# Kernel tuning notes

Measured on AMD Instinct MI355X. Metric: run time of the kernel, lower is better.

The kernel has to match this reference:

```python
import jax, jax.numpy as jnp
import numpy as np

B, D, UNITS = 32768, 1024, 1024
NB_FACTOR, SPARSITY = 3, 32
NB = D // SPARSITY  # 32 blocks of 32x32 per block-diagonal factor


def _block_t_matmul(kb, y):
    # kb: [nb, bi, bo] block-diagonal factor values; y: [nb*bi, batch]
    # computes blockdiag(kb)^T @ y without materializing the dense matrix
    nb, bi, bo = kb.shape
    yb = y.reshape(nb, bi, -1)                      # [nb, bi, batch]
    out = jnp.einsum('nio,nib->nob', kb, yb)        # [nb, bo, batch]
    return out.reshape(nb * bo, -1)


def setup_inputs() -> dict:
    key = jax.random.key(0)
    ks = jax.random.split(key, 9)
    return {
        'x': jax.random.normal(ks[0], (B, D), jnp.float32),
        'P0': jax.random.normal(ks[1], (D, D), jnp.float32),
        'P1': jax.random.normal(ks[2], (D, D), jnp.float32),
        'P2': jax.random.normal(ks[3], (D, D), jnp.float32),
        'P3': jax.random.normal(ks[4], (UNITS, UNITS), jnp.float32),
        'K0': jax.random.normal(ks[5], (NB, SPARSITY, SPARSITY), jnp.float32) * 0.05,
        'K1': jax.random.normal(ks[6], (NB, SPARSITY, SPARSITY), jnp.float32) * 0.05,
        'K2': jax.random.normal(ks[7], (NB, SPARSITY, SPARSITY), jnp.float32) * 0.05,
        'bias': jax.random.normal(ks[8], (UNITS,), jnp.float32),
    }


def reference(x, P0, P1, P2, P3, K0, K1, K2, bias):
    # output = (softmax(P3) @ Bd2^T @ softmax(P2) @ Bd1^T @ softmax(P1) @ Bd0^T @ softmax(P0) @ x^T)^T + bias
    y = x.T                                          # [D, B]
    y = jax.nn.softmax(P0, axis=1) @ y
    for kb, perm in ((K0, P1), (K1, P2), (K2, P3)):
        y = _block_t_matmul(kb, y)
        y = jax.nn.softmax(perm, axis=1) @ y
    out = y.T + bias                                 # [B, UNITS]
    return out
```

## Files before the change

kernel.cpp:

```cpp
#include <hip/hip_runtime.h>
#include <hip/hip_bf16.h>

typedef __bf16 bf16x8 __attribute__((ext_vector_type(8)));
typedef float f32x4 __attribute__((ext_vector_type(4)));
typedef unsigned short u16x8 __attribute__((ext_vector_type(8)));

__device__ __forceinline__ unsigned short f2bf(float f) {
  unsigned u = __float_as_uint(f);
  u += 0x7FFF + ((u >> 16) & 1);
  return (unsigned short)(u >> 16);
}
__device__ __forceinline__ float bf2f(unsigned short h) {
  return __uint_as_float((unsigned)h << 16);
}

__device__ __forceinline__ void gload_lds16(const void* g, void* l) {
  __builtin_amdgcn_global_load_lds(
      (const __attribute__((address_space(1))) void*)g,
      (__attribute__((address_space(3))) void*)l, 16, 0, 0);
}

#define LBAR() do { asm volatile("s_waitcnt lgkmcnt(0)" ::: "memory"); \
                    __builtin_amdgcn_s_barrier(); } while (0)

__device__ __forceinline__ void convert_slice(const float* __restrict__ x,
                                              unsigned short* __restrict__ xb,
                                              int base8, int cnt8, int cb, int nb)
{
  int i = cb * 256 + (int)threadIdx.x;
  const int stride = nb * 256;
  for (; i < cnt8; i += stride) {
    const size_t g = (size_t)(base8 + i);
    float4 v0 = ((const float4*)x)[2 * g];
    float4 v1 = ((const float4*)x)[2 * g + 1];
    u16x8 uv;
    uv[0] = f2bf(v0.x); uv[1] = f2bf(v0.y); uv[2] = f2bf(v0.z); uv[3] = f2bf(v0.w);
    uv[4] = f2bf(v1.x); uv[5] = f2bf(v1.y); uv[6] = f2bf(v1.z); uv[7] = f2bf(v1.w);
    ((u16x8*)xb)[g] = uv;
  }
}

__global__ __launch_bounds__(256)
void softmax4_kernel(const float* __restrict__ P0, const float* __restrict__ P1,
                     const float* __restrict__ P2, const float* __restrict__ P3,
                     unsigned short* __restrict__ S,
                     const float* __restrict__ cvx, unsigned short* __restrict__ cvxb,
                     int cvt_cnt)
{
  if (blockIdx.x >= 4096) {
    convert_slice(cvx, cvxb, 0, cvt_cnt, blockIdx.x - 4096, gridDim.x - 4096);
    return;
  }
  const int bid = blockIdx.x;
  const int mat = bid >> 10, row = bid & 1023;
  const float* P = (mat == 0 ? P0 : mat == 1 ? P1 : mat == 2 ? P2 : P3) + (size_t)row * 1024;
  unsigned short* out = S + ((size_t)mat << 20) + (size_t)row * 1024;
  const int t = threadIdx.x, w = t >> 6, l = t & 63;
  float4 v = ((const float4*)P)[t];
  float mx = fmaxf(fmaxf(v.x, v.y), fmaxf(v.z, v.w));
  #pragma unroll
  for (int off = 32; off > 0; off >>= 1) mx = fmaxf(mx, __shfl_xor(mx, off));
  __shared__ float redA[4], redB[4];
  if (l == 0) redA[w] = mx;
  __syncthreads();
  mx = fmaxf(fmaxf(redA[0], redA[1]), fmaxf(redA[2], redA[3]));
  float e0 = __expf(v.x - mx), e1 = __expf(v.y - mx);
  float e2 = __expf(v.z - mx), e3 = __expf(v.w - mx);
  float s = e0 + e1 + e2 + e3;
  #pragma unroll
  for (int off = 32; off > 0; off >>= 1) s += __shfl_xor(s, off);
  if (l == 0) redB[w] = s;
  __syncthreads();
  s = redB[0] + redB[1] + redB[2] + redB[3];
  float inv = 1.0f / s;
  ushort4 o;
  o.x = f2bf(e0 * inv); o.y = f2bf(e1 * inv);
  o.z = f2bf(e2 * inv); o.w = f2bf(e3 * inv);
  ((ushort4*)out)[t] = o;
}

__global__ __launch_bounds__(256)
void blockdiagT_kernel(const float* __restrict__ Kb, const unsigned short* __restrict__ in,
                       unsigned short* __restrict__ outT,
                       const float* __restrict__ cvx, unsigned short* __restrict__ cvxb,
                       int cvt_base, int cvt_cnt)
{
  if (blockIdx.x >= 128) {
    convert_slice(cvx, cvxb, cvt_base, cvt_cnt, blockIdx.x - 128, gridDim.x - 128);
    return;
  }
  const int n = blockIdx.x >> 2;
  const int c = (blockIdx.x & 3) * 256 + threadIdx.x;
  __shared__ float Ks[32][33];
  for (int t = threadIdx.x; t < 1024; t += 256)
    Ks[t >> 5][t & 31] = Kb[n * 1024 + t];
  __syncthreads();
  float ri[32];
  #pragma unroll
  for (int i = 0; i < 32; ++i)
    ri[i] = bf2f(in[(size_t)(n * 32 + i) * 1024 + c]);
  unsigned short ov[32];
  #pragma unroll
  for (int o = 0; o < 32; ++o) {
    float acc = 0.f;
    #pragma unroll
    for (int i = 0; i < 32; ++i) acc = fmaf(Ks[i][o], ri[i], acc);
    ov[o] = f2bf(acc);
  }
  u16x8* dst = (u16x8*)(outT + (size_t)c * 1024 + n * 32);
  const u16x8* src = (const u16x8*)ov;
  #pragma unroll
  for (int q = 0; q < 4; ++q) dst[q] = src[q];
}

template<int TILE, bool A_FP32, bool OUT_BIAS>
__global__ __launch_bounds__(256)
void gemm_bt_kernel(const void* __restrict__ Av, const unsigned short* __restrict__ B,
                    void* __restrict__ Cv, const float* __restrict__ bias,
                    int M, int N, int K, int nprim,
                    const float* cvx, unsigned short* cvxb, int cvt_base, int cvt_cnt)
{
  if ((int)blockIdx.x >= nprim) {
    convert_slice(cvx, cvxb, cvt_base, cvt_cnt, blockIdx.x - nprim, gridDim.x - nprim);
    return;
  }
  constexpr int FR  = TILE / 32;
  constexpr int SIT = TILE / 32;
  __shared__ unsigned short Asm[TILE * 64];
  __shared__ unsigned short Bsm[TILE * 64];
  const int tid = threadIdx.x;
  const int w = tid >> 6, l = tid & 63;
  const int bid = blockIdx.x;
  const int cpx = nprim >> 3;
  const int swz = (bid & 7) * cpx + (bid >> 3);
  const int ntn = N / TILE;
  const int n0 = (swz % ntn) * TILE;
  const int m0 = (swz / ntn) * TILE;
  const int wr = (w >> 1) * (TILE / 2), wc = (w & 1) * (TILE / 2);
  const int lr = l & 15, kg = (l >> 4) << 3;

  f32x4 acc[FR][FR] = {};
  const int KT = K >> 6;
  for (int kt = 0; kt < KT; ++kt) {
    const int k0 = kt << 6;
    if (kt) __syncthreads();
    #pragma unroll
    for (int it = 0; it < SIT; ++it) {
      int li = it * 256 + tid;
      int row = li >> 3, c8 = (li & 7) << 3;
      const unsigned short* g = B + (size_t)(n0 + row) * K + (k0 + c8);
      gload_lds16(g, (char*)Bsm + it * 4096 + w * 1024);
    }
    if (A_FP32) {
      const float* Af = (const float*)Av;
      #pragma unroll
      for (int p = 0; p < SIT; ++p) {
        int row = (tid >> 3) + p * 32;
        int c8 = (tid & 7) << 3;
        const float* g = Af + (size_t)(m0 + row) * K + (k0 + c8);
        float4 v0 = ((const float4*)g)[0];
        float4 v1 = ((const float4*)g)[1];
        u16x8 uv;
        uv[0] = f2bf(v0.x); uv[1] = f2bf(v0.y); uv[2] = f2bf(v0.z); uv[3] = f2bf(v0.w);
        uv[4] = f2bf(v1.x); uv[5] = f2bf(v1.y); uv[6] = f2bf(v1.z); uv[7] = f2bf(v1.w);
        *(u16x8*)&Asm[row * 64 + c8] = uv;
      }
    } else {
      const unsigned short* Ab = (const unsigned short*)Av;
      #pragma unroll
      for (int it = 0; it < SIT; ++it) {
        int li = it * 256 + tid;
        int row = li >> 3, c8 = (li & 7) << 3;
        const unsigned short* g = Ab + (size_t)(m0 + row) * K + (k0 + c8);
        gload_lds16(g, (char*)Asm + it * 4096 + w * 1024);
      }
    }
    __syncthreads();
    #pragma unroll
    for (int ks = 0; ks < 2; ++ks) {
      const int kb = ks * 32 + kg;
      bf16x8 af[FR], bfr[FR];
      #pragma unroll
      for (int i = 0; i < FR; ++i)
        af[i] = *(const bf16x8*)&Asm[(wr + i * 16 + lr) * 64 + kb];
      #pragma unroll
      for (int j = 0; j < FR; ++j)
        bfr[j] = *(const bf16x8*)&Bsm[(wc + j * 16 + lr) * 64 + kb];
      #pragma unroll
      for (int i = 0; i < FR; ++i)
        #pragma unroll
        for (int j = 0; j < FR; ++j)
          acc[i][j] = __builtin_amdgcn_mfma_f32_16x16x32_bf16(af[i], bfr[j], acc[i][j], 0, 0, 0);
    }
  }
  const int cr = (l >> 4) << 2;
  const int cc = l & 15;
  if (OUT_BIAS) {
    float* C = (float*)Cv;
    #pragma unroll
    for (int j = 0; j < FR; ++j) {
      int col = n0 + wc + j * 16 + cc;
      float bv = bias[col];
      #pragma unroll
      for (int i = 0; i < FR; ++i) {
        int rbase = m0 + wr + i * 16 + cr;
        #pragma unroll
        for (int r = 0; r < 4; ++r)
          C[(size_t)(rbase + r) * N + col] = acc[i][j][r] + bv;
      }
    }
  } else {
    unsigned short* C = (unsigned short*)Cv;
    #pragma unroll
    for (int j = 0; j < FR; ++j) {
      int col = n0 + wc + j * 16 + cc;
      #pragma unroll
      for (int i = 0; i < FR; ++i) {
        int rbase = m0 + wr + i * 16 + cr;
        #pragma unroll
        for (int r = 0; r < 4; ++r)
          C[(size_t)(rbase + r) * N + col] = f2bf(acc[i][j][r]);
      }
    }
  }
}

template<int QI, int QJ>
__device__ __forceinline__ void phase_compute(const char* Ab, const char* Bb,
    int wm, int wn, int lr, int klo, int sw, f32x4 (&accq)[4][2])
{
  const char* Ah = Ab + QI * 16384;
  const char* Bh = Bb + QJ * 16384;
  #pragma unroll
  for (int ks = 0; ks < 2; ++ks) {
    const int cb = (ks * 64 + klo) ^ sw;
    bf16x8 av[4], bv[2];
    #pragma unroll
    for (int i = 0; i < 4; ++i) {
      const int ra = wm * 64 + i * 16 + lr;
      av[i] = *(const bf16x8*)(Ah + ra * 128 + cb);
    }
    #pragma unroll
    for (int j = 0; j < 2; ++j) {
      const int rb = wn * 32 + j * 16 + lr;
      bv[j] = *(const bf16x8*)(Bh + rb * 128 + cb);
    }
    __builtin_amdgcn_s_setprio(1);
    #pragma unroll
    for (int i = 0; i < 4; ++i)
      #pragma unroll
      for (int j = 0; j < 2; ++j)
        accq[i][j] = __builtin_amdgcn_mfma_f32_16x16x32_bf16(av[i], bv[j], accq[i][j], 0, 0, 0);
    __builtin_amdgcn_s_setprio(0);
  }
}

__global__ __launch_bounds__(512, 2)
void gemm256_kernel(const unsigned short* __restrict__ A,
                    const unsigned short* __restrict__ B,
                    float* __restrict__ C, const float* __restrict__ bias,
                    int N, int K)
{
  extern __shared__ __align__(16) char lds[];
  const int tid = threadIdx.x;
  const int w = tid >> 6, l = tid & 63;
  const int wm = w >> 2, wn = w & 3;
  const int lr = l & 15;
  const int klo = (l >> 4) << 4;
  const int sw  = (lr & 7) << 4;

  const int nwg = gridDim.x;
  const int bid = blockIdx.x;
  const int cpx = nwg >> 3;
  const int swz = (bid & 7) * cpx + (bid >> 3);
  const int ntn = N >> 8;
  const int n0 = (swz % ntn) << 8;
  const int m0 = (swz / ntn) << 8;

  unsigned int aoff[2][2], boff[2][2];
  #pragma unroll
  for (int q = 0; q < 2; ++q)
    #pragma unroll
    for (int it = 0; it < 2; ++it) {
      int L = it * 8192 + tid * 16;
      int r = L >> 7;
      int cs = (L & 127) ^ ((r & 7) << 4);
      aoff[q][it] = (unsigned)(m0 + q * 128 + r) * K + (cs >> 1);
      boff[q][it] = (unsigned)(n0 + q * 128 + r) * K + (cs >> 1);
    }
  char* ldsA = lds;
  char* ldsB = lds + 65536;
  const int wdst = w * 1024;

#define STG_A(bufo, q, k0) do { \
    gload_lds16(A + aoff[q][0] + (k0), ldsA + (bufo) + (q) * 16384 + wdst); \
    gload_lds16(A + aoff[q][1] + (k0), ldsA + (bufo) + (q) * 16384 + 8192 + wdst); } while (0)
#define STG_B(bufo, q, k0) do { \
    gload_lds16(B + boff[q][0] + (k0), ldsB + (bufo) + (q) * 16384 + wdst); \
    gload_lds16(B + boff[q][1] + (k0), ldsB + (bufo) + (q) * 16384 + 8192 + wdst); } while (0)

  f32x4 acc[2][2][4][2] = {};

  STG_A(0, 0, 0); STG_B(0, 0, 0); STG_B(0, 1, 0); STG_A(0, 1, 0);

  const int NT = K >> 6;
  int curo = 0;
  for (int t = 0; t < NT - 1; ++t) {
    const int nxto = curo ^ 32768;
    const int k1 = (t + 1) << 6;
    STG_A(nxto, 0, k1);
    asm volatile("s_waitcnt vmcnt(6)" ::: "memory");
    LBAR();
    phase_compute<0, 0>(ldsA + curo, ldsB + curo, wm, wn, lr, klo, sw, acc[0][0]);
    STG_B(nxto, 0, k1);
    asm volatile("s_waitcnt vmcnt(6)" ::: "memory");
    LBAR();
    phase_compute<0, 1>(ldsA + curo, ldsB + curo, wm, wn, lr, klo, sw, acc[0][1]);
    STG_B(nxto, 1, k1);
    asm volatile("s_waitcnt vmcnt(6)" ::: "memory");
    LBAR();
    phase_compute<1, 0>(ldsA + curo, ldsB + curo, wm, wn, lr, klo, sw, acc[1][0]);
    STG_A(nxto, 1, k1);
    phase_compute<1, 1>(ldsA + curo, ldsB + curo, wm, wn, lr, klo, sw, acc[1][1]);
    curo = nxto;
  }
  asm volatile("s_waitcnt vmcnt(4)" ::: "memory");
  LBAR();
  phase_compute<0, 0>(ldsA + curo, ldsB + curo, wm, wn, lr, klo, sw, acc[0][0]);
  asm volatile("s_waitcnt vmcnt(2)" ::: "memory");
  LBAR();
  phase_compute<0, 1>(ldsA + curo, ldsB + curo, wm, wn, lr, klo, sw, acc[0][1]);
  asm volatile("s_waitcnt vmcnt(0)" ::: "memory");
  LBAR();
  phase_compute<1, 0>(ldsA + curo, ldsB + curo, wm, wn, lr, klo, sw, acc[1][0]);
  phase_compute<1, 1>(ldsA + curo, ldsB + curo, wm, wn, lr, klo, sw, acc[1][1]);

  const int cr = (l >> 4) << 2;
  const int cc = l & 15;
  #pragma unroll
  for (int qi = 0; qi < 2; ++qi)
    #pragma unroll
    for (int qj = 0; qj < 2; ++qj)
      #pragma unroll
      for (int j = 0; j < 2; ++j) {
        const int col = n0 + qj * 128 + wn * 32 + j * 16 + cc;
        const float bv = bias[col];
        #pragma unroll
        for (int i = 0; i < 4; ++i) {
          const int rbase = m0 + qi * 128 + wm * 64 + i * 16 + cr;
          #pragma unroll
          for (int r = 0; r < 4; ++r)
            C[(size_t)(rbase + r) * N + col] = acc[qi][qj][i][j][r] + bv;
        }
      }
#undef STG_A
#undef STG_B
}

extern "C" void kernel_launch(void* const* d_in, const int* in_sizes, int n_in,
                              void* d_out, int out_size, void* d_ws, size_t ws_size,
                              hipStream_t stream) {
  (void)in_sizes; (void)n_in; (void)out_size;
  const float* x    = (const float*)d_in[0];
  const float* P0   = (const float*)d_in[1];
  const float* P1   = (const float*)d_in[2];
  const float* P2   = (const float*)d_in[3];
  const float* P3   = (const float*)d_in[4];
  const float* K0   = (const float*)d_in[5];
  const float* K1   = (const float*)d_in[6];
  const float* K2   = (const float*)d_in[7];
  const float* bias = (const float*)d_in[8];

  unsigned short* S  = (unsigned short*)d_ws;
  unsigned short* T0 = S + (size_t)4 * (1u << 20);
  unsigned short* T1 = T0 + (1u << 20);
  unsigned short* Xb = T1 + (1u << 20);
  const size_t need = ((size_t)6 * (1u << 20) + (size_t)32768 * 1024) * 2;
  const bool have_xb = ws_size >= need;
  unsigned short* xbp = have_xb ? Xb : nullptr;

  const int SL = 524288;
  const int smx_cvt = have_xb ? 2 * SL : 0;
  const int smx_grid = 4096 + (have_xb ? 1024 : 0);
  const int bd_grid  = 128 + (have_xb ? 512 : 0);
  const int g64_grid = 256 + (have_xb ? 512 : 0);
  const int g64_cvt  = have_xb ? SL : 0;

  softmax4_kernel<<<smx_grid, 256, 0, stream>>>(P0, P1, P2, P3, S, x, xbp, smx_cvt);

  const unsigned short* S0 = S;
  const unsigned short* S1 = S + (1u << 20);
  const unsigned short* S2 = S + (2u << 20);
  const unsigned short* S3 = S + (3u << 20);

  blockdiagT_kernel<<<bd_grid, 256, 0, stream>>>(K0, S0, T0, x, xbp, 2 * SL, g64_cvt);
  gemm_bt_kernel<64, false, false><<<g64_grid, 256, 0, stream>>>((const void*)S1, T0,
      (void*)T1, nullptr, 1024, 1024, 1024, 256, x, xbp, 3 * SL, g64_cvt);
  blockdiagT_kernel<<<bd_grid, 256, 0, stream>>>(K1, T1, T0, x, xbp, 4 * SL, g64_cvt);
  gemm_bt_kernel<64, false, false><<<g64_grid, 256, 0, stream>>>((const void*)S2, T0,
      (void*)T1, nullptr, 1024, 1024, 1024, 256, x, xbp, 5 * SL, g64_cvt);
  blockdiagT_kernel<<<bd_grid, 256, 0, stream>>>(K2, T1, T0, x, xbp, 6 * SL, g64_cvt);
  gemm_bt_kernel<64, false, false><<<g64_grid, 256, 0, stream>>>((const void*)S3, T0,
      (void*)T1, nullptr, 1024, 1024, 1024, 256, x, xbp, 7 * SL, g64_cvt);

  bool ok256 = false;
  if (have_xb) {
    hipError_t e = hipFuncSetAttribute((const void*)gemm256_kernel,
                                       hipFuncAttributeMaxDynamicSharedMemorySize, 131072);
    ok256 = (e == hipSuccess);
  }
  if (ok256) {
    gemm256_kernel<<<512, 512, 131072, stream>>>(Xb, T1, (float*)d_out, bias, 1024, 1024);
  } else if (have_xb) {
    gemm_bt_kernel<128, false, true><<<2048, 256, 0, stream>>>((const void*)Xb, T1,
        d_out, bias, 32768, 1024, 1024, 2048, nullptr, nullptr, 0, 0);
  } else {
    gemm_bt_kernel<128, true, true><<<2048, 256, 0, stream>>>((const void*)x, T1,
        d_out, bias, 32768, 1024, 1024, 2048, nullptr, nullptr, 0, 0);
  }
}
```

Before: 191.0 us.

## Reassociate weight-chain products to pair independent stages into dual launches

The dense 1024x1024 weight chain is now evaluated by reassociation, multiplying pairs of factors concurrently (blockdiag with S2 and S0 together, then two GEMMs in one launch) instead of a strict right-to-left sequence. A new right-multiply block-diagonal kernel handles the middle factor from the other side. This cuts the number of serial kernel launches in the small-matrix prelude and doubles per-launch parallelism on the 1024-sized steps, while keeping the bf16 convert slices spread across launches. It relies on associativity, which changes bf16 rounding order.

```diff
diff --git a/kernel.cpp b/kernel.cpp
--- a/kernel.cpp
+++ b/kernel.cpp
@@ -79,18 +79,12 @@
   ((ushort4*)out)[t] = o;
 }
 
-__global__ __launch_bounds__(256)
-void blockdiagT_kernel(const float* __restrict__ Kb, const unsigned short* __restrict__ in,
-                       unsigned short* __restrict__ outT,
-                       const float* __restrict__ cvx, unsigned short* __restrict__ cvxb,
-                       int cvt_base, int cvt_cnt)
-{
-  if (blockIdx.x >= 128) {
-    convert_slice(cvx, cvxb, cvt_base, cvt_cnt, blockIdx.x - 128, gridDim.x - 128);
-    return;
-  }
-  const int n = blockIdx.x >> 2;
-  const int c = (blockIdx.x & 3) * 256 + threadIdx.x;
+__device__ __forceinline__ void bdT_body(const float* __restrict__ Kb,
+                                         const unsigned short* __restrict__ in,
+                                         unsigned short* __restrict__ outT, int bid)
+{
+  const int n = bid >> 2;
+  const int c = (bid & 3) * 256 + threadIdx.x;
   __shared__ float Ks[32][33];
   for (int t = threadIdx.x; t < 1024; t += 256)
     Ks[t >> 5][t & 31] = Kb[n * 1024 + t];
@@ -113,24 +107,70 @@
   for (int q = 0; q < 4; ++q) dst[q] = src[q];
 }
 
+__global__ __launch_bounds__(256)
+void blockdiagT_dual_kernel(const float* Ka, const unsigned short* ina, unsigned short* outa,
+                            const float* Kb2, const unsigned short* inb, unsigned short* outb,
+                            const float* cvx, unsigned short* cvxb, int cvt_base, int cvt_cnt)
+{
+  const int bid = blockIdx.x;
+  if (bid >= 256) {
+    convert_slice(cvx, cvxb, cvt_base, cvt_cnt, bid - 256, gridDim.x - 256);
+    return;
+  }
+  const bool sec = bid >= 128;
+  bdT_body(sec ? Kb2 : Ka, sec ? inb : ina, sec ? outb : outa, sec ? bid - 128 : bid);
+}
+
+__global__ __launch_bounds__(256)
+void bdiag_right_kernel(const float* __restrict__ Kb, const unsigned short* __restrict__ Yt,
+                        unsigned short* __restrict__ Zt,
+                        const float* cvx, unsigned short* cvxb, int cvt_base, int cvt_cnt)
+{
+  const int bid = blockIdx.x;
+  if (bid >= 256) {
+    convert_slice(cvx, cvxb, cvt_base, cvt_cnt, bid - 256, gridDim.x - 256);
+    return;
+  }
+  const int n = bid & 31, rowg = bid >> 5;
+  __shared__ float Ks[32][32];
+  for (int t = threadIdx.x; t < 1024; t += 256)
+    Ks[t >> 5][t & 31] = Kb[n * 1024 + t];
+  __syncthreads();
+  const int row = rowg * 128 + ((int)threadIdx.x >> 1);
+  const int ih = ((int)threadIdx.x & 1) * 16;
+  const unsigned short* yrow = Yt + (size_t)row * 1024 + n * 32;
+  float y[32];
+  #pragma unroll
+  for (int q = 0; q < 4; ++q) {
+    u16x8 v = ((const u16x8*)yrow)[q];
+    #pragma unroll
+    for (int e = 0; e < 8; ++e) y[q * 8 + e] = bf2f(v[e]);
+  }
+  float acc[16] = {};
+  #pragma unroll
+  for (int o = 0; o < 32; ++o)
+    #pragma unroll
+    for (int ii = 0; ii < 16; ++ii)
+      acc[ii] = fmaf(y[o], Ks[o][ih + ii], acc[ii]);
+  u16x8 ov[2];
+  #pragma unroll
+  for (int ii = 0; ii < 16; ++ii) ov[ii >> 3][ii & 7] = f2bf(acc[ii]);
+  u16x8* dst = (u16x8*)(Zt + (size_t)row * 1024 + n * 32 + ih);
+  dst[0] = ov[0]; dst[1] = ov[1];
+}
+
 template<int TILE, bool A_FP32, bool OUT_BIAS>
-__global__ __launch_bounds__(256)
-void gemm_bt_kernel(const void* __restrict__ Av, const unsigned short* __restrict__ B,
-                    void* __restrict__ Cv, const float* __restrict__ bias,
-                    int M, int N, int K, int nprim,
-                    const float* cvx, unsigned short* cvxb, int cvt_base, int cvt_cnt)
-{
-  if ((int)blockIdx.x >= nprim) {
-    convert_slice(cvx, cvxb, cvt_base, cvt_cnt, blockIdx.x - nprim, gridDim.x - nprim);
-    return;
-  }
+__device__ __forceinline__ void gemm_body(const void* __restrict__ Av,
+                                          const unsigned short* __restrict__ B,
+                                          void* __restrict__ Cv, const float* __restrict__ bias,
+                                          int N, int K, int nprim, int bid)
+{
   constexpr int FR  = TILE / 32;
   constexpr int SIT = TILE / 32;
   __shared__ unsigned short Asm[TILE * 64];
   __shared__ unsigned short Bsm[TILE * 64];
   const int tid = threadIdx.x;
   const int w = tid >> 6, l = tid & 63;
-  const int bid = blockIdx.x;
   const int cpx = nprim >> 3;
   const int swz = (bid & 7) * cpx + (bid >> 3);
   const int ntn = N / TILE;
@@ -223,6 +263,35 @@
       }
     }
   }
+}
+
+template<int TILE, bool A_FP32, bool OUT_BIAS>
+__global__ __launch_bounds__(256)
+void gemm_bt_kernel(const void* __restrict__ Av, const unsigned short* __restrict__ B,
+                    void* __restrict__ Cv, const float* __restrict__ bias,
+                    int N, int K, int nprim,
+                    const float* cvx, unsigned short* cvxb, int cvt_base, int cvt_cnt)
+{
+  if ((int)blockIdx.x >= nprim) {
+    convert_slice(cvx, cvxb, cvt_base, cvt_cnt, blockIdx.x - nprim, gridDim.x - nprim);
+    return;
+  }
+  gemm_body<TILE, A_FP32, OUT_BIAS>(Av, B, Cv, bias, N, K, nprim, blockIdx.x);
+}
+
+__global__ __launch_bounds__(256)
+void gemm_dual_kernel(const unsigned short* A0, const unsigned short* B0, unsigned short* C0,
+                      const unsigned short* A1, const unsigned short* B1, unsigned short* C1,
+                      const float* cvx, unsigned short* cvxb, int cvt_base, int cvt_cnt)
+{
+  const int bid = blockIdx.x;
+  if (bid >= 512) {
+    convert_slice(cvx, cvxb, cvt_base, cvt_cnt, bid - 512, gridDim.x - 512);
+    return;
+  }
+  const bool sec = bid >= 256;
+  gemm_body<64, false, false>(sec ? A1 : A0, sec ? B1 : B0, sec ? (void*)C1 : (void*)C0,
+                              nullptr, 1024, 1024, 256, sec ? bid - 256 : bid);
 }
 
 template<int QI, int QJ>
@@ -372,36 +441,36 @@
   const float* bias = (const float*)d_in[8];
 
   unsigned short* S  = (unsigned short*)d_ws;
-  unsigned short* T0 = S + (size_t)4 * (1u << 20);
-  unsigned short* T1 = T0 + (1u << 20);
-  unsigned short* Xb = T1 + (1u << 20);
+  unsigned short* s0 = S;
+  unsigned short* s1 = S + (1u << 20);
+  unsigned short* s2 = S + (2u << 20);
+  unsigned short* s3 = S + (3u << 20);
+  unsigned short* t0 = S + (4u << 20);
+  unsigned short* t1 = S + (5u << 20);
+  unsigned short* Xb = S + (6u << 20);
   const size_t need = ((size_t)6 * (1u << 20) + (size_t)32768 * 1024) * 2;
   const bool have_xb = ws_size >= need;
   unsigned short* xbp = have_xb ? Xb : nullptr;
 
   const int SL = 524288;
-  const int smx_cvt = have_xb ? 2 * SL : 0;
-  const int smx_grid = 4096 + (have_xb ? 1024 : 0);
-  const int bd_grid  = 128 + (have_xb ? 512 : 0);
-  const int g64_grid = 256 + (have_xb ? 512 : 0);
-  const int g64_cvt  = have_xb ? SL : 0;
-
-  softmax4_kernel<<<smx_grid, 256, 0, stream>>>(P0, P1, P2, P3, S, x, xbp, smx_cvt);
-
-  const unsigned short* S0 = S;
-  const unsigned short* S1 = S + (1u << 20);
-  const unsigned short* S2 = S + (2u << 20);
-  const unsigned short* S3 = S + (3u << 20);
-
-  blockdiagT_kernel<<<bd_grid, 256, 0, stream>>>(K0, S0, T0, x, xbp, 2 * SL, g64_cvt);
-  gemm_bt_kernel<64, false, false><<<g64_grid, 256, 0, stream>>>((const void*)S1, T0,
-      (void*)T1, nullptr, 1024, 1024, 1024, 256, x, xbp, 3 * SL, g64_cvt);
-  blockdiagT_kernel<<<bd_grid, 256, 0, stream>>>(K1, T1, T0, x, xbp, 4 * SL, g64_cvt);
-  gemm_bt_kernel<64, false, false><<<g64_grid, 256, 0, stream>>>((const void*)S2, T0,
-      (void*)T1, nullptr, 1024, 1024, 1024, 256, x, xbp, 5 * SL, g64_cvt);
-  blockdiagT_kernel<<<bd_grid, 256, 0, stream>>>(K2, T1, T0, x, xbp, 6 * SL, g64_cvt);
-  gemm_bt_kernel<64, false, false><<<g64_grid, 256, 0, stream>>>((const void*)S3, T0,
-      (void*)T1, nullptr, 1024, 1024, 1024, 256, x, xbp, 7 * SL, g64_cvt);
+  const int cvt2 = have_xb ? 2 * SL : 0;
+  const int cvt1 = have_xb ? SL : 0;
+  const int tail_smx = have_xb ? 1024 : 0;
+  const int tail_512 = have_xb ? 512 : 0;
+  const int tail_256 = have_xb ? 256 : 0;
+
+  softmax4_kernel<<<4096 + tail_smx, 256, 0, stream>>>(P0, P1, P2, P3, S, x, xbp, cvt2);
+
+  blockdiagT_dual_kernel<<<256 + tail_512, 256, 0, stream>>>(K2, s2, t0, K0, s0, t1,
+                                                             x, xbp, 2 * SL, cvt2);
+
+  gemm_dual_kernel<<<512 + tail_512, 256, 0, stream>>>(s3, t0, s0, t1, s1, s2,
+                                                       x, xbp, 4 * SL, cvt2);
+
+  bdiag_right_kernel<<<256 + tail_256, 256, 0, stream>>>(K1, s2, t1, x, xbp, 6 * SL, cvt1);
+
+  gemm_bt_kernel<64, false, false><<<256 + tail_512, 256, 0, stream>>>((const void*)s0, t1,
+      (void*)t0, nullptr, 1024, 1024, 256, x, xbp, 7 * SL, cvt1);
 
   bool ok256 = false;
   if (have_xb) {
@@ -410,12 +479,12 @@
     ok256 = (e == hipSuccess);
   }
   if (ok256) {
-    gemm256_kernel<<<512, 512, 131072, stream>>>(Xb, T1, (float*)d_out, bias, 1024, 1024);
+    gemm256_kernel<<<512, 512, 131072, stream>>>(Xb, t0, (float*)d_out, bias, 1024, 1024);
   } else if (have_xb) {
-    gemm_bt_kernel<128, false, true><<<2048, 256, 0, stream>>>((const void*)Xb, T1,
-        d_out, bias, 32768, 1024, 1024, 2048, nullptr, nullptr, 0, 0);
+    gemm_bt_kernel<128, false, true><<<2048, 256, 0, stream>>>((const void*)Xb, t0,
+        d_out, bias, 1024, 1024, 2048, nullptr, nullptr, 0, 0);
   } else {
-    gemm_bt_kernel<128, true, true><<<2048, 256, 0, stream>>>((const void*)x, T1,
-        d_out, bias, 32768, 1024, 1024, 2048, nullptr, nullptr, 0, 0);
-  }
-}
+    gemm_bt_kernel<128, true, true><<<2048, 256, 0, stream>>>((const void*)x, t0,
+        d_out, bias, 1024, 1024, 2048, nullptr, nullptr, 0, 0);
+  }
+}
```

New measurement: 161.2 us. 15.6% less time.
